# Performance work log

Measured on AMD Instinct MI355X. Metric: run time of the kernel, lower is better.

## Reference

```python
import jax, jax.numpy as jnp
import numpy as np

N_HEADS, N_KV, HEAD_DIM = 16, 4, 64
DIM = 4096
LATENT = N_HEADS * HEAD_DIM   # 1024
KV_DIM = N_KV * HEAD_DIM      # 256
KSZ = 3


def _causal_conv1d(x, w, b, groups):
    # x: [B,S,C]; w: [Cout, Cin//groups, K]; causal left padding (K-1)
    y = jax.lax.conv_general_dilated(
        x.transpose(0, 2, 1), w, window_strides=(1,),
        padding=[(w.shape[-1] - 1, 0)], feature_group_count=groups,
        dimension_numbers=('NCH', 'OIH', 'NCH'))
    return (y + b[None, :, None]).transpose(0, 2, 1)


def _rope(x, cos, sin):
    # x: [B,H,S,D] interleaved pairs; cos/sin: [1,1,S,D//2]
    x1, x2 = x[..., ::2], x[..., 1::2]
    out = jnp.stack([x1 * cos - x2 * sin, x1 * sin + x2 * cos], axis=-1)
    return out.reshape(x.shape)


def _l2norm(x):
    n = jnp.sqrt(jnp.sum(x * x, axis=-1, keepdims=True))
    return x / jnp.maximum(n, 1e-12)


def setup_inputs() -> dict:
    key = jax.random.key(0)
    ks = jax.random.split(key, 12)
    sc = 0.02
    x = jax.random.normal(ks[0], (2, 2048, DIM), jnp.float32)
    w_qkv = jax.random.normal(ks[1], (LATENT + 2 * KV_DIM, DIM), jnp.float32) * sc
    w_o = jax.random.normal(ks[2], (DIM, LATENT), jnp.float32) * sc
    qc1_w = jax.random.normal(ks[3], (LATENT, LATENT // N_HEADS, KSZ), jnp.float32) * sc
    qc1_b = jnp.zeros((LATENT,), jnp.float32)
    qc2_w = jax.random.normal(ks[4], (LATENT, LATENT, KSZ), jnp.float32) * sc
    qc2_b = jnp.zeros((LATENT,), jnp.float32)
    kc1_w = jax.random.normal(ks[5], (KV_DIM, KV_DIM // N_KV, KSZ), jnp.float32) * sc
    kc1_b = jnp.zeros((KV_DIM,), jnp.float32)
    kc2_w = jax.random.normal(ks[6], (KV_DIM, KV_DIM, KSZ), jnp.float32) * sc
    kc2_b = jnp.zeros((KV_DIM,), jnp.float32)
    key_temp = jnp.full((1,), float(HEAD_DIM) ** 0.5, jnp.float32)
    return dict(x=x, w_qkv=w_qkv, w_o=w_o, qc1_w=qc1_w, qc1_b=qc1_b,
                qc2_w=qc2_w, qc2_b=qc2_b, kc1_w=kc1_w, kc1_b=kc1_b,
                kc2_w=kc2_w, kc2_b=kc2_b, key_temp=key_temp)


def _forward(x, w_qkv, w_o, qc1_w, qc1_b, qc2_w, qc2_b, kc1_w, kc1_b, kc2_w, kc2_b, key_temp):
    B, S, _ = x.shape
    qkv = x @ w_qkv.T  # [B,S,LATENT+2*KV_DIM]
    q = qkv[..., :LATENT]
    k = qkv[..., LATENT:LATENT + KV_DIM]
    # value shift: first half current token, second half previous token (0 at t=0)
    half = KV_DIM // 2
    v_curr = qkv[..., LATENT + KV_DIM:LATENT + KV_DIM + half]
    v_prev = qkv[..., LATENT + KV_DIM + half:]
    v = jnp.concatenate([v_curr, jnp.pad(v_prev[:, :-1, :], ((0, 0), (1, 0), (0, 0)))], axis=-1)
    q_pre, k_pre = q, k
    # grouped causal conv sequences on q and k
    q = _causal_conv1d(_causal_conv1d(q, qc1_w, qc1_b, N_HEADS), qc2_w, qc2_b, 1)
    k = _causal_conv1d(_causal_conv1d(k, kc1_w, kc1_b, N_KV), kc2_w, kc2_b, 1)
    # qk-mean coupling (n_groups = 4 branch)
    q_mean = q_pre.reshape(B, S, N_HEADS, HEAD_DIM).mean(axis=2)  # [B,S,hd]
    k_mean = k_pre.reshape(B, S, N_KV, HEAD_DIM).mean(axis=2)
    q = q.reshape(B, S, N_HEADS, HEAD_DIM) + 0.5 * k_mean[:, :, None, :]
    k = k.reshape(B, S, N_KV, HEAD_DIM) + 0.5 * q_mean[:, :, None, :]
    q = q.transpose(0, 2, 1, 3)                                   # [B,H,S,d]
    k = k.transpose(0, 2, 1, 3)                                   # [B,Hkv,S,d]
    v = v.reshape(B, S, N_KV, HEAD_DIM).transpose(0, 2, 1, 3)
    # qk-norm with learned key temperature
    q = _l2norm(q)
    k = _l2norm(k) * key_temp
    # RoPE (interleaved pairs)
    inv = 1.0 / (10000.0 ** (jnp.arange(0, HEAD_DIM, 2, dtype=jnp.float32) / HEAD_DIM))
    ang = jnp.arange(S, dtype=jnp.float32)[:, None] * inv[None, :]  # [S,d/2]
    cos, sin = jnp.cos(ang)[None, None], jnp.sin(ang)[None, None]
    q = _rope(q, cos, sin)
    k = _rope(k, cos, sin)
    # GQA: each kv head repeated n_groups times contiguously
    kg = jnp.repeat(k, N_HEADS // N_KV, axis=1)
    vg = jnp.repeat(v, N_HEADS // N_KV, axis=1)
    scale = HEAD_DIM ** -0.5
    scores = jnp.einsum('bhqd,bhkd->bhqk', q, kg) * scale
    causal = jnp.tril(jnp.ones((S, S), dtype=bool))
    scores = jnp.where(causal[None, None], scores, jnp.finfo(scores.dtype).min)
    attn = jax.nn.softmax(scores, axis=-1)
    out = jnp.einsum('bhqk,bhkd->bhqd', attn, vg)
    out = out.transpose(0, 2, 1, 3).reshape(B, S, LATENT)
    return out @ w_o.T  # output_scale = 1.0


def reference(x, w_qkv, w_o, qc1_w, qc1_b, qc2_w, qc2_b, kc1_w, kc1_b, kc2_w, kc2_b, key_temp):
    return _forward(x, w_qkv, w_o, qc1_w, qc1_b, qc2_w, qc2_b, kc1_w, kc1_b, kc2_w, kc2_b, key_temp)
```

## Files before the change

kernel.cpp:

```cpp
#include <hip/hip_runtime.h>
#include <hip/hip_bf16.h>
#include <cstddef>

#define NB 2
#define SEQ 2048
#define DIMX 4096
#define NH 16
#define NKV 4
#define HD 64
#define LATENT 1024
#define KVD 256
#define QKVN 1536
#define BS (NB*SEQ)
#define SP (SEQ+2)

typedef __attribute__((ext_vector_type(8))) short short8v;
typedef __attribute__((ext_vector_type(4))) float f32x4;
typedef __attribute__((ext_vector_type(4))) unsigned short ushort4v;
typedef __attribute__((ext_vector_type(4))) unsigned int uint4v;

static __device__ __forceinline__ unsigned short f2bf(float f) {
    union { float f; unsigned u; } v; v.f = f;
    unsigned r = v.u + 0x7fffu + ((v.u >> 16) & 1u);
    return (unsigned short)(r >> 16);
}

static __device__ __forceinline__ unsigned cvt_pk_bf16(float lo, float hi) {
    unsigned r;
    asm("v_cvt_pk_bf16_f32 %0, %1, %2" : "=v"(r) : "v"(lo), "v"(hi));
    return r;
}

static __device__ __forceinline__ void gload_lds16(const unsigned short* g, unsigned short* l) {
    __builtin_amdgcn_global_load_lds((const __attribute__((address_space(1))) void*)g,
                                     (__attribute__((address_space(3))) void*)l, 16, 0, 0);
}

__global__ __launch_bounds__(256)
void cast_f2b(const float* __restrict__ in, unsigned short* __restrict__ out, int n4)
{
    const int i = blockIdx.x * 256 + threadIdx.x;
    if (i < n4) {
        const float4 v = *reinterpret_cast<const float4*>(in + (size_t)i * 4);
        ushort4v o = {f2bf(v.x), f2bf(v.y), f2bf(v.z), f2bf(v.w)};
        *reinterpret_cast<ushort4v*>(out + (size_t)i * 4) = o;
    }
}

__global__ __launch_bounds__(256)
void w3reorder(const float* __restrict__ w, unsigned short* __restrict__ wr, int O, int I)
{
    const int idx = blockIdx.x * 256 + threadIdx.x;
    if (idx < O * I * 3) {
        const int o = idx / (I * 3), rem = idx % (I * 3);
        const int j = rem / I, c = rem % I;
        wr[idx] = f2bf(w[(size_t)o * I * 3 + c * 3 + j]);
    }
}

__global__ __launch_bounds__(256)
void zero_pad(unsigned short* __restrict__ pq, unsigned short* __restrict__ pk)
{
    const int t = blockIdx.x * 256 + threadIdx.x;
    if (t < 2 * 2 * LATENT) {
        const int b = t / (2 * LATENT), r = (t % (2 * LATENT)) / LATENT, c = t % LATENT;
        pq[((size_t)b * SP + r) * LATENT + c] = 0;
    }
    if (t < 2 * 2 * KVD) {
        const int b = t / (2 * KVD), r = (t % (2 * KVD)) / KVD, c = t % KVD;
        pk[((size_t)b * SP + r) * KVD + c] = 0;
    }
}

__global__ __launch_bounds__(256)
void add2(const float* __restrict__ p0, const float* __restrict__ p1,
          const float* __restrict__ bias, float* __restrict__ out, int n4, int ncols)
{
    const int i = blockIdx.x * 256 + threadIdx.x;
    if (i < n4) {
        const float4 a = *reinterpret_cast<const float4*>(p0 + (size_t)i * 4);
        const float4 b = *reinterpret_cast<const float4*>(p1 + (size_t)i * 4);
        float4 o = make_float4(a.x + b.x, a.y + b.y, a.z + b.z, a.w + b.w);
        if (bias != nullptr) {
            const int col = (i * 4) % ncols;
            o.x += bias[col]; o.y += bias[col + 1]; o.z += bias[col + 2]; o.w += bias[col + 3];
        }
        *reinterpret_cast<float4*>(out + (size_t)i * 4) = o;
    }
}

template<int CONV>
__global__ __launch_bounds__(256)
void gemm_bf16(const unsigned short* __restrict__ A, const unsigned short* __restrict__ W,
               const float* __restrict__ bias, float* __restrict__ C,
               int M, int N, int K, int Cch, int klen, size_t pstride)
{
    __shared__ unsigned short Abuf[2][128 * 32];
    __shared__ unsigned short Bbuf[2][128 * 32];
    const int gx = gridDim.x;
    const int nwg = gx * gridDim.y;
    const int lin = blockIdx.y * gx + blockIdx.x;
    const int swz = (lin & 7) * (nwg >> 3) + (lin >> 3);
    const int n0 = (swz % gx) * 128, m0 = (swz / gx) * 128;
    const int koff = blockIdx.z * klen;
    C += (size_t)blockIdx.z * pstride;
    const int tid = threadIdx.x;
    const int wave = tid >> 6, lane = tid & 63;
    const int lg = lane >> 4, lr = lane & 15;
    const int wm = (wave & 1) * 64, wn = (wave >> 1) * 64;
    const int sr = wave * 32 + (lane >> 2);
    const int sc = (lane & 3) * 8;
    const int bb = m0 / SEQ, s0 = m0 % SEQ;

    const int NT = klen / 32;
    f32x4 acc[4][4];
    #pragma unroll
    for (int i = 0; i < 4; i++)
        #pragma unroll
        for (int j = 0; j < 4; j++) acc[i][j] = (f32x4){0.f, 0.f, 0.f, 0.f};

    auto stage = [&](int buf, int kt) {
        const int k0 = koff + kt * 32;
        const unsigned short* ga0;
        if (!CONV) {
            ga0 = A + (size_t)(m0 + sr) * K + k0 + sc;
        } else {
            const int j = k0 / Cch, c0 = k0 - j * Cch;
            ga0 = A + (size_t)(bb * SP + s0 + j + sr) * Cch + c0 + sc;
        }
        const unsigned short* gb0 = W + (size_t)(n0 + sr) * K + k0 + sc;
        const size_t astep = (size_t)16 * (CONV ? Cch : K);
        #pragma unroll
        for (int i = 0; i < 2; i++) {
            gload_lds16(ga0 + i * astep, &Abuf[buf][(wave * 2 + i) * 512]);
            gload_lds16(gb0 + (size_t)i * 16 * K, &Bbuf[buf][(wave * 2 + i) * 512]);
        }
    };

    stage(0, 0);
    __syncthreads();
    int cur = 0;
    for (int kt = 0; kt < NT; ++kt) {
        if (kt + 1 < NT) stage(cur ^ 1, kt + 1);
        short8v af[4], bf[4];
        #pragma unroll
        for (int mi = 0; mi < 4; mi++)
            af[mi] = *reinterpret_cast<const short8v*>(&Abuf[cur][(wm + mi * 16 + lr) * 32 + lg * 8]);
        #pragma unroll
        for (int ni = 0; ni < 4; ni++)
            bf[ni] = *reinterpret_cast<const short8v*>(&Bbuf[cur][(wn + ni * 16 + lr) * 32 + lg * 8]);
        #pragma unroll
        for (int mi = 0; mi < 4; mi++)
            #pragma unroll
            for (int ni = 0; ni < 4; ni++)
                acc[mi][ni] = __builtin_amdgcn_mfma_f32_16x16x32_bf16(af[mi], bf[ni], acc[mi][ni], 0, 0, 0);
        __syncthreads();
        cur ^= 1;
    }

    #pragma unroll
    for (int ni = 0; ni < 4; ni++) {
        const int col = n0 + wn + ni * 16 + lr;
        const float bv = bias ? bias[col] : 0.f;
        #pragma unroll
        for (int mi = 0; mi < 4; mi++)
            #pragma unroll
            for (int r = 0; r < 4; r++)
                C[(size_t)(m0 + wm + mi * 16 + lg * 4 + r) * N + col] = acc[mi][ni][r] + bv;
    }
}

__global__ __launch_bounds__(256)
void conv1_grouped(const float* __restrict__ qkv, int coloff,
                   const float* __restrict__ w, const float* __restrict__ bias,
                   unsigned short* __restrict__ out, int CH)
{
    const int t0 = blockIdx.x * 64;
    const int b  = blockIdx.y;
    const int g  = blockIdx.z;
    __shared__ float xs[66][64];
    for (int idx = threadIdx.x; idx < 66 * 64; idx += 256) {
        const int i = idx >> 6, ic = idx & 63;
        const int tt = t0 + i - 2;
        xs[i][ic] = (tt >= 0) ? qkv[(size_t)(b * SEQ + tt) * QKVN + coloff + g * 64 + ic] : 0.f;
    }
    __syncthreads();
    const int oc = threadIdx.x & 63;
    const int ibase = (threadIdx.x >> 6) * 16;
    float acc[16];
    const float bv = bias[g * 64 + oc];
    #pragma unroll
    for (int i = 0; i < 16; i++) acc[i] = bv;
    const float* wp = w + (size_t)(g * 64 + oc) * 192;
    for (int ic = 0; ic < 64; ic++) {
        const float w0 = wp[ic * 3 + 0], w1 = wp[ic * 3 + 1], w2 = wp[ic * 3 + 2];
        float xv[18];
        #pragma unroll
        for (int r = 0; r < 18; r++) xv[r] = xs[ibase + r][ic];
        #pragma unroll
        for (int i = 0; i < 16; i++) acc[i] += w0 * xv[i] + w1 * xv[i + 1] + w2 * xv[i + 2];
    }
    #pragma unroll
    for (int i = 0; i < 16; i++)
        out[((size_t)b * SP + 2 + t0 + ibase + i) * CH + g * 64 + oc] = f2bf(acc[i]);
}

__global__ __launch_bounds__(64)
void meanv_kernel(const float* __restrict__ qkv, float* __restrict__ qmean,
                  float* __restrict__ kmean, unsigned short* __restrict__ vRow)
{
    const int t = blockIdx.x, d = threadIdx.x;
    const int b = t >> 11, s = t & (SEQ - 1);
    const float* row = qkv + (size_t)t * QKVN;
    float qs = 0.f;
    #pragma unroll
    for (int h = 0; h < NH; h++) qs += row[h * 64 + d];
    qmean[t * 64 + d] = qs * (1.f / NH);
    float ks = 0.f;
    #pragma unroll
    for (int h = 0; h < NKV; h++) ks += row[LATENT + h * 64 + d];
    kmean[t * 64 + d] = ks * (1.f / NKV);
    #pragma unroll
    for (int g = 0; g < NKV; g++) {
        const int c = g * 64 + d;
        float v;
        if (c < 128) v = row[LATENT + KVD + c];
        else         v = (s > 0) ? qkv[(size_t)(t - 1) * QKVN + LATENT + KVD + 128 + (c - 128)] : 0.f;
        vRow[((size_t)(b * NKV + g) * SEQ + s) * 64 + d] = f2bf(v);
    }
}

__global__ __launch_bounds__(256)
void vtrans(const unsigned short* __restrict__ vRow, unsigned short* __restrict__ vTb)
{
    const int s0 = blockIdx.x * 64;
    const int bg = blockIdx.y;
    __shared__ unsigned short t[64][72];
    const int tid = threadIdx.x;
    {
        const int r = tid >> 2, c0 = (tid & 3) * 16;
        const unsigned short* p = vRow + ((size_t)bg * SEQ + s0 + r) * 64 + c0;
        const short8v a = *reinterpret_cast<const short8v*>(p);
        const short8v bv = *reinterpret_cast<const short8v*>(p + 8);
        #pragma unroll
        for (int j = 0; j < 8; j++) { t[r][c0 + j] = (unsigned short)a[j]; t[r][c0 + 8 + j] = (unsigned short)bv[j]; }
    }
    __syncthreads();
    {
        const int d = tid >> 2, ss = (tid & 3) * 16;
        short8v o0, o1;
        #pragma unroll
        for (int j = 0; j < 8; j++) { o0[j] = (short)t[ss + j][d]; o1[j] = (short)t[ss + 8 + j][d]; }
        unsigned short* op = vTb + ((size_t)bg * 64 + d) * SEQ + s0 + ss;
        *reinterpret_cast<short8v*>(op) = o0;
        *reinterpret_cast<short8v*>(op + 8) = o1;
    }
}

__global__ __launch_bounds__(64)
void qk_final(const float* __restrict__ qc2a, const float* __restrict__ qc2b,
              const float* __restrict__ kc2a, const float* __restrict__ kc2b,
              const float* __restrict__ qbias, const float* __restrict__ kbias,
              const float* __restrict__ qmean, const float* __restrict__ kmean,
              const float* __restrict__ key_temp,
              unsigned short* __restrict__ qTb, unsigned short* __restrict__ kTb)
{
    const int t = blockIdx.x, hh = blockIdx.y, d = threadIdx.x;
    const int b = t >> 11, s = t & (SEQ - 1);
    float val;
    if (hh < NH) {
        const size_t off = (size_t)t * LATENT + hh * 64 + d;
        val = qc2a[off] + qc2b[off] + qbias[hh * 64 + d] + 0.5f * kmean[t * 64 + d];
    } else {
        const size_t off = (size_t)t * KVD + (hh - NH) * 64 + d;
        val = kc2a[off] + kc2b[off] + kbias[(hh - NH) * 64 + d] + 0.5f * qmean[t * 64 + d];
    }
    float ss = val * val;
    #pragma unroll
    for (int off = 32; off >= 1; off >>= 1) ss += __shfl_xor(ss, off);
    const float n = sqrtf(ss);
    val = val / fmaxf(n, 1e-12f);
    if (hh >= NH) val *= key_temp[0];
    const int i = d >> 1;
    const float inv = powf(10000.f, -(float)(2 * i) * (1.f / HD));
    const float ang = (float)s * inv;
    const float cv = cosf(ang), sv = sinf(ang);
    const float partner = __shfl_xor(val, 1);
    const float x1 = (d & 1) ? partner : val;
    const float x2 = (d & 1) ? val : partner;
    const float o = (d & 1) ? (x1 * sv + x2 * cv) : (x1 * cv - x2 * sv);
    if (hh < NH) qTb[((size_t)(b * NH + hh) * SEQ + s) * 64 + d] = f2bf(o);
    else         kTb[((size_t)(b * NKV + (hh - NH)) * SEQ + s) * 64 + d] = f2bf(o);
}

__global__ __launch_bounds__(256)
void attn_mfma(const unsigned short* __restrict__ qTb, const unsigned short* __restrict__ kTb,
               const unsigned short* __restrict__ vTb, unsigned short* __restrict__ attn_out)
{
    const int wg = blockIdx.x;
    int bh, blk;
    if (wg < 256) {
        const int xcd = wg & 7, i = wg >> 3;
        bh = (xcd << 2) | (i >> 3);
        blk = 15 - (i & 7);
    } else {
        const int u = wg - 256;
        const int xcd = u & 7, i = u >> 3;
        bh = (xcd << 2) | (i >> 3);
        blk = i & 7;
    }
    const int b = bh >> 4, h = bh & 15, g = h >> 2;
    const int tid = threadIdx.x;
    const int wave = tid >> 6, lane = tid & 63;
    const int lg = lane >> 4, lr = lane & 15;
    const int qt = blk * 4 + wave;
    const int q0 = qt * 32;
    const int ctot = (blk + 1) * 4;

    __shared__ __align__(16) unsigned short SB[2][8][512];

    short8v qf[2][2];
    const unsigned short* qbase = qTb + ((size_t)(b * NH + h) * SEQ + q0) * 64;
    #pragma unroll
    for (int mf = 0; mf < 2; mf++)
        #pragma unroll
        for (int dc = 0; dc < 2; dc++)
            qf[mf][dc] = *reinterpret_cast<const short8v*>(qbase + (size_t)(mf * 16 + lr) * 64 + dc * 32 + lg * 8);

    f32x4 acc[2][4];
    float lsum[2] = {0.f, 0.f};
    #pragma unroll
    for (int mf = 0; mf < 2; mf++)
        #pragma unroll
        for (int dt = 0; dt < 4; dt++) acc[mf][dt] = (f32x4){0.f, 0.f, 0.f, 0.f};

    const unsigned short* kbase = kTb + (size_t)(b * NKV + g) * SEQ * 64;
    const unsigned short* vbase = vTb + (size_t)(b * NKV + g) * 64 * SEQ;
    const float EC = 0.125f * 1.44269504f;
    const int src01 = ((lg & 1) << 5) + lr;
    const int src23 = src01 + 16;
    const bool hi = (lg >= 2);

    auto stage = [&](int buf, int c) {
        const int k0 = c * 32;
        #pragma unroll
        for (int i = 0; i < 2; i++) {
            const int ch = wave * 2 + i;
            const unsigned short* src;
            if (ch < 4) src = kbase + (size_t)(k0 + (ch >> 1) * 16 + lr) * 64 + (ch & 1) * 32 + lg * 8;
            else        src = vbase + (size_t)((ch - 4) * 16 + lr) * SEQ + k0 + lg * 8;
            gload_lds16(src, &SB[buf][ch][lane * 8]);
        }
    };

    stage(0, 0);
    __syncthreads();
    int cur = 0;
    for (int c = 0; c < ctot; ++c) {
        if (c + 1 < ctot) stage(cur ^ 1, c + 1);
        if (c <= qt) {
            const int k0 = c * 32;
            short8v kf[2][2], vf[4];
            #pragma unroll
            for (int kt = 0; kt < 2; kt++)
                #pragma unroll
                for (int dc = 0; dc < 2; dc++)
                    kf[kt][dc] = *reinterpret_cast<const short8v*>(&SB[cur][kt * 2 + dc][lane * 8]);
            #pragma unroll
            for (int dt = 0; dt < 4; dt++)
                vf[dt] = *reinterpret_cast<const short8v*>(&SB[cur][4 + dt][lane * 8]);

            const bool diag = (c == qt);
            #pragma unroll
            for (int mf = 0; mf < 2; mf++) {
                f32x4 z0 = (f32x4){0.f, 0.f, 0.f, 0.f}, z1 = (f32x4){0.f, 0.f, 0.f, 0.f};
                z0 = __builtin_amdgcn_mfma_f32_16x16x32_bf16(kf[0][0], qf[mf][0], z0, 0, 0, 0);
                z0 = __builtin_amdgcn_mfma_f32_16x16x32_bf16(kf[0][1], qf[mf][1], z0, 0, 0, 0);
                z1 = __builtin_amdgcn_mfma_f32_16x16x32_bf16(kf[1][0], qf[mf][0], z1, 0, 0, 0);
                z1 = __builtin_amdgcn_mfma_f32_16x16x32_bf16(kf[1][1], qf[mf][1], z1, 0, 0, 0);
                float p0[4], p1[4];
                #pragma unroll
                for (int r = 0; r < 4; r++) {
                    p0[r] = exp2f(z0[r] * EC);
                    p1[r] = exp2f(z1[r] * EC);
                }
                if (diag) {
                    const int q = q0 + mf * 16 + lr;
                    #pragma unroll
                    for (int r = 0; r < 4; r++) {
                        if (k0 + 4 * lg + r > q)      p0[r] = 0.f;
                        if (k0 + 16 + 4 * lg + r > q) p1[r] = 0.f;
                    }
                }
                lsum[mf] += (p0[0] + p0[1]) + (p0[2] + p0[3]) + (p1[0] + p1[1]) + (p1[2] + p1[3]);
                const unsigned W00 = cvt_pk_bf16(p0[0], p0[1]);
                const unsigned W01 = cvt_pk_bf16(p0[2], p0[3]);
                const unsigned W10 = cvt_pk_bf16(p1[0], p1[1]);
                const unsigned W11 = cvt_pk_bf16(p1[2], p1[3]);
                const unsigned a0 = __shfl(W00, src01), b0 = __shfl(W10, src01);
                const unsigned a1 = __shfl(W01, src01), b1 = __shfl(W11, src01);
                const unsigned a2 = __shfl(W00, src23), b2 = __shfl(W10, src23);
                const unsigned a3 = __shfl(W01, src23), b3 = __shfl(W11, src23);
                uint4v pw;
                pw.x = hi ? b0 : a0;
                pw.y = hi ? b1 : a1;
                pw.z = hi ? b2 : a2;
                pw.w = hi ? b3 : a3;
                const short8v pa = __builtin_bit_cast(short8v, pw);
                #pragma unroll
                for (int dt = 0; dt < 4; dt++)
                    acc[mf][dt] = __builtin_amdgcn_mfma_f32_16x16x32_bf16(pa, vf[dt], acc[mf][dt], 0, 0, 0);
            }
        }
        __syncthreads();
        cur ^= 1;
    }

    float den[2];
    #pragma unroll
    for (int mf = 0; mf < 2; mf++) {
        float s = lsum[mf];
        s += __shfl_xor(s, 16); s += __shfl_xor(s, 32);
        den[mf] = s;
    }

    #pragma unroll
    for (int mf = 0; mf < 2; mf++) {
        float dinv[4];
        #pragma unroll
        for (int r = 0; r < 4; r++) dinv[r] = 1.f / __shfl(den[mf], 4 * lg + r);
        #pragma unroll
        for (int dt = 0; dt < 4; dt++)
            #pragma unroll
            for (int r = 0; r < 4; r++) {
                const int q = q0 + mf * 16 + 4 * lg + r;
                attn_out[(size_t)(b * SEQ + q) * LATENT + h * 64 + dt * 16 + lr] = f2bf(acc[mf][dt][r] * dinv[r]);
            }
    }
}

extern "C" void kernel_launch(void* const* d_in, const int* in_sizes, int n_in,
                              void* d_out, int out_size, void* d_ws, size_t ws_size,
                              hipStream_t stream)
{
    const float* x       = (const float*)d_in[0];
    const float* w_qkv   = (const float*)d_in[1];
    const float* w_o     = (const float*)d_in[2];
    const float* qc1_w   = (const float*)d_in[3];
    const float* qc1_b   = (const float*)d_in[4];
    const float* qc2_w   = (const float*)d_in[5];
    const float* qc2_b   = (const float*)d_in[6];
    const float* kc1_w   = (const float*)d_in[7];
    const float* kc1_b   = (const float*)d_in[8];
    const float* kc2_w   = (const float*)d_in[9];
    const float* kc2_b   = (const float*)d_in[10];
    const float* key_temp = (const float*)d_in[11];

    char* wsb = (char*)d_ws;
    float* qkv = (float*)wsb;                 wsb += (size_t)BS * QKVN * 4;
    float* qc2 = qkv;
    float* kc2 = (float*)((char*)qkv + (size_t)BS * LATENT * 4);
    unsigned short* pq  = (unsigned short*)wsb;  wsb += (size_t)NB * SP * LATENT * 2;
    unsigned short* pk  = (unsigned short*)wsb;  wsb += (size_t)NB * SP * KVD * 2;
    float* qmean = (float*)wsb;  wsb += (size_t)BS * HD * 4;
    float* kmean = (float*)wsb;  wsb += (size_t)BS * HD * 4;
    unsigned short* qTb  = (unsigned short*)wsb;  wsb += (size_t)BS * LATENT * 2;
    unsigned short* kTb  = (unsigned short*)wsb;  wsb += (size_t)BS * KVD * 2;
    unsigned short* vRow = (unsigned short*)wsb;  wsb += (size_t)BS * KVD * 2;
    unsigned short* vTb  = (unsigned short*)wsb;  wsb += (size_t)BS * KVD * 2;
    unsigned short* xb   = (unsigned short*)wsb;  wsb += (size_t)BS * DIMX * 2;
    unsigned short* attnb  = xb;
    unsigned short* qc2wr  = (unsigned short*)((char*)xb + (size_t)BS * LATENT * 2);
    unsigned short* kc2wr  = (unsigned short*)((char*)qc2wr + (size_t)LATENT * LATENT * 3 * 2);
    unsigned short* wqkvb = (unsigned short*)wsb;  wsb += (size_t)QKVN * DIMX * 2;
    unsigned short* wob   = wqkvb;

    const size_t QKV_PS = (size_t)BS * QKVN;
    float* qc2p1 = (float*)((char*)d_ws + 67512320);
    float* kc2p1 = (float*)((char*)d_ws + (size_t)BS * QKVN * 4);
    const size_t QC2_PS = (size_t)(qc2p1 - qc2);
    const size_t KC2_PS = (size_t)(kc2p1 - kc2);

    float* outp = (float*)d_out;

    cast_f2b<<<dim3(BS * DIMX / 4 / 256), 256, 0, stream>>>(x, xb, BS * DIMX / 4);
    cast_f2b<<<dim3(QKVN * DIMX / 4 / 256), 256, 0, stream>>>(w_qkv, wqkvb, QKVN * DIMX / 4);
    gemm_bf16<0><<<dim3(QKVN / 128, BS / 128, 2), 256, 0, stream>>>(xb, wqkvb, nullptr, qkv, BS, QKVN, DIMX, 0, DIMX / 2, QKV_PS);
    add2<<<dim3(BS * QKVN / 4 / 256), 256, 0, stream>>>(qkv, qkv + QKV_PS, nullptr, qkv, BS * QKVN / 4, 4);
    cast_f2b<<<dim3(DIMX * LATENT / 4 / 256), 256, 0, stream>>>(w_o, wob, DIMX * LATENT / 4);
    w3reorder<<<dim3((LATENT * LATENT * 3 + 255) / 256), 256, 0, stream>>>(qc2_w, qc2wr, LATENT, LATENT);
    w3reorder<<<dim3((KVD * KVD * 3 + 255) / 256), 256, 0, stream>>>(kc2_w, kc2wr, KVD, KVD);
    meanv_kernel<<<dim3(BS), 64, 0, stream>>>(qkv, qmean, kmean, vRow);
    vtrans<<<dim3(SEQ / 64, NB * NKV), 256, 0, stream>>>(vRow, vTb);
    zero_pad<<<dim3(16), 256, 0, stream>>>(pq, pk);
    conv1_grouped<<<dim3(SEQ / 64, NB, NH),  256, 0, stream>>>(qkv, 0,      qc1_w, qc1_b, pq, LATENT);
    conv1_grouped<<<dim3(SEQ / 64, NB, NKV), 256, 0, stream>>>(qkv, LATENT, kc1_w, kc1_b, pk, KVD);
    gemm_bf16<1><<<dim3(LATENT / 128, BS / 128, 2), 256, 0, stream>>>(pq, qc2wr, nullptr, qc2, BS, LATENT, LATENT * 3, LATENT, LATENT * 3 / 2, QC2_PS);
    gemm_bf16<1><<<dim3(KVD / 128, BS / 128, 2), 256, 0, stream>>>(pk, kc2wr, nullptr, kc2, BS, KVD, KVD * 3, KVD, KVD * 3 / 2, KC2_PS);
    qk_final<<<dim3(BS, NH + NKV), 64, 0, stream>>>(qc2, qc2p1, kc2, kc2p1, qc2_b, kc2_b,
                                                    qmean, kmean, key_temp, qTb, kTb);
    attn_mfma<<<dim3(512), 256, 0, stream>>>(qTb, kTb, vTb, attnb);
    gemm_bf16<0><<<dim3(DIMX / 128, BS / 128, 1), 256, 0, stream>>>(attnb, wob, nullptr, outp, BS, DIMX, LATENT, 0, LATENT, 0);
}
```

Before: 394.1 us.

## Stage 64-key chunks in attention, add MFMA priority, precompute RoPE table

The attention kernel now stages 64 keys (two 32-key sub-tiles) per double-buffered LDS step. This halves the number of barriers per pass at the cost of twice the shared memory. MFMA sections are wrapped in s_setprio to favour the matrix issue. RoPE cos/sin values are precomputed once into a table stored in the now-free vRow buffer, replacing per-element powf/sinf/cosf in qk_final. The extra LDS may lower occupancy, and the table reuses a buffer that vtrans has already consumed.

```diff
diff --git a/kernel.cpp b/kernel.cpp
--- a/kernel.cpp
+++ b/kernel.cpp
@@ -87,6 +87,16 @@
         }
         *reinterpret_cast<float4*>(out + (size_t)i * 4) = o;
     }
+}
+
+__global__ __launch_bounds__(256)
+void rope_tab(float2* __restrict__ tab)
+{
+    const int idx = blockIdx.x * 256 + threadIdx.x;
+    const int s = idx >> 5, i = idx & 31;
+    const float inv = powf(10000.f, -(float)(2 * i) * (1.f / HD));
+    const float ang = (float)s * inv;
+    tab[idx] = make_float2(cosf(ang), sinf(ang));
 }
 
 template<int CONV>
@@ -262,7 +272,7 @@
               const float* __restrict__ kc2a, const float* __restrict__ kc2b,
               const float* __restrict__ qbias, const float* __restrict__ kbias,
               const float* __restrict__ qmean, const float* __restrict__ kmean,
-              const float* __restrict__ key_temp,
+              const float* __restrict__ key_temp, const float2* __restrict__ rtab,
               unsigned short* __restrict__ qTb, unsigned short* __restrict__ kTb)
 {
     const int t = blockIdx.x, hh = blockIdx.y, d = threadIdx.x;
@@ -281,10 +291,8 @@
     const float n = sqrtf(ss);
     val = val / fmaxf(n, 1e-12f);
     if (hh >= NH) val *= key_temp[0];
-    const int i = d >> 1;
-    const float inv = powf(10000.f, -(float)(2 * i) * (1.f / HD));
-    const float ang = (float)s * inv;
-    const float cv = cosf(ang), sv = sinf(ang);
+    const float2 cs = rtab[s * 32 + (d >> 1)];
+    const float cv = cs.x, sv = cs.y;
     const float partner = __shfl_xor(val, 1);
     const float x1 = (d & 1) ? partner : val;
     const float x2 = (d & 1) ? val : partner;
@@ -315,9 +323,9 @@
     const int lg = lane >> 4, lr = lane & 15;
     const int qt = blk * 4 + wave;
     const int q0 = qt * 32;
-    const int ctot = (blk + 1) * 4;
-
-    __shared__ __align__(16) unsigned short SB[2][8][512];
+    const int ctot2 = (blk + 1) * 2;
+
+    __shared__ __align__(16) unsigned short SB[2][16][512];
 
     short8v qf[2][2];
     const unsigned short* qbase = qTb + ((size_t)(b * NH + h) * SEQ + q0) * 64;
@@ -341,43 +349,50 @@
     const int src23 = src01 + 16;
     const bool hi = (lg >= 2);
 
-    auto stage = [&](int buf, int c) {
-        const int k0 = c * 32;
-        #pragma unroll
-        for (int i = 0; i < 2; i++) {
-            const int ch = wave * 2 + i;
+    auto stage64 = [&](int buf, int cc) {
+        const int kb = cc * 64;
+        #pragma unroll
+        for (int i = 0; i < 4; i++) {
+            const int ch = wave * 4 + i;
+            const int st = ch >> 3, chl = ch & 7;
+            const int k0 = kb + st * 32;
             const unsigned short* src;
-            if (ch < 4) src = kbase + (size_t)(k0 + (ch >> 1) * 16 + lr) * 64 + (ch & 1) * 32 + lg * 8;
-            else        src = vbase + (size_t)((ch - 4) * 16 + lr) * SEQ + k0 + lg * 8;
+            if (chl < 4) src = kbase + (size_t)(k0 + (chl >> 1) * 16 + lr) * 64 + (chl & 1) * 32 + lg * 8;
+            else         src = vbase + (size_t)((chl - 4) * 16 + lr) * SEQ + k0 + lg * 8;
             gload_lds16(src, &SB[buf][ch][lane * 8]);
         }
     };
 
-    stage(0, 0);
+    stage64(0, 0);
     __syncthreads();
     int cur = 0;
-    for (int c = 0; c < ctot; ++c) {
-        if (c + 1 < ctot) stage(cur ^ 1, c + 1);
-        if (c <= qt) {
+    for (int cc = 0; cc < ctot2; ++cc) {
+        if (cc + 1 < ctot2) stage64(cur ^ 1, cc + 1);
+        #pragma unroll
+        for (int st = 0; st < 2; ++st) {
+            const int c = cc * 2 + st;
+            if (c > qt) continue;
             const int k0 = c * 32;
             short8v kf[2][2], vf[4];
             #pragma unroll
             for (int kt = 0; kt < 2; kt++)
                 #pragma unroll
                 for (int dc = 0; dc < 2; dc++)
-                    kf[kt][dc] = *reinterpret_cast<const short8v*>(&SB[cur][kt * 2 + dc][lane * 8]);
+                    kf[kt][dc] = *reinterpret_cast<const short8v*>(&SB[cur][st * 8 + kt * 2 + dc][lane * 8]);
             #pragma unroll
             for (int dt = 0; dt < 4; dt++)
-                vf[dt] = *reinterpret_cast<const short8v*>(&SB[cur][4 + dt][lane * 8]);
+                vf[dt] = *reinterpret_cast<const short8v*>(&SB[cur][st * 8 + 4 + dt][lane * 8]);
 
             const bool diag = (c == qt);
             #pragma unroll
             for (int mf = 0; mf < 2; mf++) {
                 f32x4 z0 = (f32x4){0.f, 0.f, 0.f, 0.f}, z1 = (f32x4){0.f, 0.f, 0.f, 0.f};
+                __builtin_amdgcn_s_setprio(1);
                 z0 = __builtin_amdgcn_mfma_f32_16x16x32_bf16(kf[0][0], qf[mf][0], z0, 0, 0, 0);
                 z0 = __builtin_amdgcn_mfma_f32_16x16x32_bf16(kf[0][1], qf[mf][1], z0, 0, 0, 0);
                 z1 = __builtin_amdgcn_mfma_f32_16x16x32_bf16(kf[1][0], qf[mf][0], z1, 0, 0, 0);
                 z1 = __builtin_amdgcn_mfma_f32_16x16x32_bf16(kf[1][1], qf[mf][1], z1, 0, 0, 0);
+                __builtin_amdgcn_s_setprio(0);
                 float p0[4], p1[4];
                 #pragma unroll
                 for (int r = 0; r < 4; r++) {
@@ -407,9 +422,11 @@
                 pw.z = hi ? b2 : a2;
                 pw.w = hi ? b3 : a3;
                 const short8v pa = __builtin_bit_cast(short8v, pw);
+                __builtin_amdgcn_s_setprio(1);
                 #pragma unroll
                 for (int dt = 0; dt < 4; dt++)
                     acc[mf][dt] = __builtin_amdgcn_mfma_f32_16x16x32_bf16(pa, vf[dt], acc[mf][dt], 0, 0, 0);
+                __builtin_amdgcn_s_setprio(0);
             }
         }
         __syncthreads();
@@ -480,6 +497,7 @@
     float* kc2p1 = (float*)((char*)d_ws + (size_t)BS * QKVN * 4);
     const size_t QC2_PS = (size_t)(qc2p1 - qc2);
     const size_t KC2_PS = (size_t)(kc2p1 - kc2);
+    float2* rtab = (float2*)vRow;
 
     float* outp = (float*)d_out;
 
@@ -492,13 +510,14 @@
     w3reorder<<<dim3((KVD * KVD * 3 + 255) / 256), 256, 0, stream>>>(kc2_w, kc2wr, KVD, KVD);
     meanv_kernel<<<dim3(BS), 64, 0, stream>>>(qkv, qmean, kmean, vRow);
     vtrans<<<dim3(SEQ / 64, NB * NKV), 256, 0, stream>>>(vRow, vTb);
+    rope_tab<<<dim3(SEQ * 32 / 256), 256, 0, stream>>>(rtab);
     zero_pad<<<dim3(16), 256, 0, stream>>>(pq, pk);
     conv1_grouped<<<dim3(SEQ / 64, NB, NH),  256, 0, stream>>>(qkv, 0,      qc1_w, qc1_b, pq, LATENT);
     conv1_grouped<<<dim3(SEQ / 64, NB, NKV), 256, 0, stream>>>(qkv, LATENT, kc1_w, kc1_b, pk, KVD);
     gemm_bf16<1><<<dim3(LATENT / 128, BS / 128, 2), 256, 0, stream>>>(pq, qc2wr, nullptr, qc2, BS, LATENT, LATENT * 3, LATENT, LATENT * 3 / 2, QC2_PS);
     gemm_bf16<1><<<dim3(KVD / 128, BS / 128, 2), 256, 0, stream>>>(pk, kc2wr, nullptr, kc2, BS, KVD, KVD * 3, KVD, KVD * 3 / 2, KC2_PS);
     qk_final<<<dim3(BS, NH + NKV), 64, 0, stream>>>(qc2, qc2p1, kc2, kc2p1, qc2_b, kc2_b,
-                                                    qmean, kmean, key_temp, qTb, kTb);
+                                                    qmean, kmean, key_temp, rtab, qTb, kTb);
     attn_mfma<<<dim3(512), 256, 0, stream>>>(qTb, kTb, vTb, attnb);
     gemm_bf16<0><<<dim3(DIMX / 128, BS / 128, 1), 256, 0, stream>>>(attnb, wob, nullptr, outp, BS, DIMX, LATENT, 0, LATENT, 0);
 }
```

After: 382.3 us. 3.0% less time.
